# Kernel tuning notes

Hardware: AMD Instinct MI355X
Metric: run time of the kernel (lower is better)

## Reference

```python
import jax, jax.numpy as jnp
import numpy as np

Q_CHAN = 8          # q_chan
IN_CHAN = 128
KS = 56             # kernel_size; ks*ks must equal h*w
STRIDE = 2
BN_EPS = 1e-5


def setup_inputs() -> dict:
    key = jax.random.key(0)
    ks = jax.random.split(key, 10)
    n, c, h, w = 4, IN_CHAN, 56, 56
    hw = h * w  # 3136 == KS*KS
    oc = 4 * Q_CHAN  # qkv conv output channels = 32
    return {
        "x": jax.random.normal(ks[0], (n, c, h, w), dtype=jnp.float32),
        # 1x1 conv weight (out_ch, in_ch) and bias
        "w_qkv": jax.random.normal(ks[1], (oc, c), dtype=jnp.float32) * (1.0 / np.sqrt(c)),
        "b_qkv": jnp.zeros((oc,), dtype=jnp.float32),
        # BatchNorm (inference mode) affine + running stats
        "bn_gamma": jnp.ones((oc,), dtype=jnp.float32),
        "bn_beta": jnp.zeros((oc,), dtype=jnp.float32),
        "bn_mean": jnp.zeros((oc,), dtype=jnp.float32),
        "bn_var": jnp.ones((oc,), dtype=jnp.float32),
        # learned relative position biases, trailing dim = ks*ks = h*w
        "rq": jax.random.normal(ks[2], (Q_CHAN, KS * KS), dtype=jnp.float32),
        "rk": jax.random.normal(ks[3], (Q_CHAN, KS * KS), dtype=jnp.float32),
        "rv": jax.random.normal(ks[4], (2 * Q_CHAN, KS * KS), dtype=jnp.float32),
    }


def reference(x, w_qkv, b_qkv, bn_gamma, bn_beta, bn_mean, bn_var, rq, rk, rv):
    n, c, h, w = x.shape
    # 1x1 conv + inference BatchNorm
    qkv = jnp.einsum('nchw,oc->nohw', x, w_qkv) + b_qkv[None, :, None, None]
    scale = bn_gamma / jnp.sqrt(bn_var + BN_EPS)
    qkv = (qkv - bn_mean[None, :, None, None]) * scale[None, :, None, None] + bn_beta[None, :, None, None]
    qkv = qkv.reshape(n, 4 * Q_CHAN, h * w)
    q = qkv[:, :Q_CHAN]            # [n, 8, hw]
    k = qkv[:, Q_CHAN:2 * Q_CHAN]  # [n, 8, hw]
    v = qkv[:, 2 * Q_CHAN:]        # [n, 16, hw]
    # global attention scores with learned positional bias terms: [n, hw, hw]
    sc = (jnp.einsum('nci,ncj->nij', q, k)
          + jnp.einsum('ci,ncj->nij', rq, q)
          + jnp.einsum('ci,ncj->nij', rk, k))
    sc = jax.nn.softmax(sc, axis=2)
    v = v + rv[None]
    out = jnp.einsum('nij,ncj->nci', sc, v).reshape(n, 2 * Q_CHAN, h, w)
    # AvgPool2d(kernel=stride, stride=stride)
    s = STRIDE
    out = out.reshape(n, 2 * Q_CHAN, h // s, s, w // s, s).mean(axis=(3, 5))
    return out
```

## Files before the change

### kernel.cpp

```cpp
#include <hip/hip_runtime.h>

#define HW 3136
#define CIN 128
#define MHAT 40.0f
#define NSEV 7
#define LOG2E 1.44269504088896340736f
#define NEGC  (-57.7078018f)

typedef __attribute__((ext_vector_type(8))) short bf16x8;
typedef __attribute__((ext_vector_type(4))) float f32x4;

__device__ __forceinline__ unsigned cvtpk(float a, float b) {
    unsigned r;
    asm("v_cvt_pk_bf16_f32 %0, %1, %2" : "=v"(r) : "v"(a), "v"(b));
    return r;
}
__device__ __forceinline__ float lo2f(unsigned p) { return __uint_as_float(p << 16); }
__device__ __forceinline__ float hi2f(unsigned p) { return __uint_as_float(p & 0xffff0000u); }
__device__ __forceinline__ float exp2_hw(float x) {
    float r;
    asm("v_exp_f32 %0, %1" : "=v"(r) : "v"(x));
    return r;
}

union UF { bf16x8 v; unsigned u[4]; };


__global__ __launch_bounds__(256) void proj_mfma(
    const float* __restrict__ x, const float* __restrict__ w,
    const float* __restrict__ bq, const float* __restrict__ gm,
    const float* __restrict__ bt, const float* __restrict__ mu,
    const float* __restrict__ vr, const float* __restrict__ rq,
    const float* __restrict__ rk, const float* __restrict__ rv,
    short* __restrict__ QKWS, short* __restrict__ ASQB, short* __restrict__ VWS)
{
    const int tid = threadIdx.x;
    const int wv = tid >> 6, lane = tid & 63;
    const int il = lane & 15, q = lane >> 4;
    const int jb = blockIdx.x * 64;
    const int nn = blockIdx.y;
    const int z  = blockIdx.z;
    const int jA = jb + wv * 16 + il;
    const float* xn = x + (size_t)nn * CIN * HW;

    UF xh[4], xl[4];
    #pragma unroll
    for (int s = 0; s < 4; ++s) {
        float xv[8];
        #pragma unroll
        for (int u = 0; u < 8; ++u)
            xv[u] = xn[(size_t)(s * 32 + q * 8 + u) * HW + jA];
        #pragma unroll
        for (int t = 0; t < 4; ++t) {
            unsigned hp = cvtpk(xv[2 * t], xv[2 * t + 1]);
            unsigned lp = cvtpk(xv[2 * t] - lo2f(hp), xv[2 * t + 1] - hi2f(hp));
            xh[s].u[t] = hp;
            xl[s].u[t] = lp;
        }
    }
    UF wh[4], wl[4];
    const float* wp = w + (size_t)(z * 16 + il) * CIN;
    #pragma unroll
    for (int s = 0; s < 4; ++s) {
        float4 f0 = *(const float4*)(wp + s * 32 + q * 8);
        float4 f1 = *(const float4*)(wp + s * 32 + q * 8 + 4);
        float wf[8] = {f0.x, f0.y, f0.z, f0.w, f1.x, f1.y, f1.z, f1.w};
        #pragma unroll
        for (int t = 0; t < 4; ++t) {
            unsigned hp = cvtpk(wf[2 * t], wf[2 * t + 1]);
            unsigned lp = cvtpk(wf[2 * t] - lo2f(hp), wf[2 * t + 1] - hi2f(hp));
            wh[s].u[t] = hp;
            wl[s].u[t] = lp;
        }
    }

    f32x4 a0 = {0.f, 0.f, 0.f, 0.f}, a1 = {0.f, 0.f, 0.f, 0.f};
    if (z == 0) {
        #pragma unroll
        for (int s = 0; s < 4; ++s) a0 = __builtin_amdgcn_mfma_f32_16x16x32_bf16(wh[s].v, xh[s].v, a0, 0, 0, 0);
        #pragma unroll
        for (int s = 0; s < 4; ++s) a1 = __builtin_amdgcn_mfma_f32_16x16x32_bf16(wl[s].v, xh[s].v, a1, 0, 0, 0);
        #pragma unroll
        for (int s = 0; s < 4; ++s) a1 = __builtin_amdgcn_mfma_f32_16x16x32_bf16(wh[s].v, xl[s].v, a1, 0, 0, 0);
    } else {
        #pragma unroll
        for (int s = 0; s < 4; ++s) a0 = __builtin_amdgcn_mfma_f32_16x16x32_bf16(xh[s].v, wh[s].v, a0, 0, 0, 0);
        #pragma unroll
        for (int s = 0; s < 4; ++s) a1 = __builtin_amdgcn_mfma_f32_16x16x32_bf16(xl[s].v, wh[s].v, a1, 0, 0, 0);
        #pragma unroll
        for (int s = 0; s < 4; ++s) a1 = __builtin_amdgcn_mfma_f32_16x16x32_bf16(xh[s].v, wl[s].v, a1, 0, 0, 0);
    }
    const f32x4 d = a0 + a1;

    if (z == 0) {
        const int jj = jA;
        float hv[4], av[4];
        #pragma unroll
        for (int r = 0; r < 4; ++r) {
            const int ch = q * 4 + r;
            const float sc = gm[ch] * rsqrtf(vr[ch] + 1e-5f);
            const float sh = (bq[ch] - mu[ch]) * sc + bt[ch];
            const float val = d[r] * sc + sh;
            hv[r] = val;
            const float a = (ch < 8) ? (val + rk[(size_t)ch * HW + jj])
                                     : rq[(size_t)(ch - 8) * HW + jj];
            av[r] = a * LOG2E;
        }
        short* qrow = QKWS + ((size_t)nn * HW + jj) * 32;
        short* arow = ASQB + ((size_t)nn * HW + jj) * 32;
        const int pb = (q * 4) ^ 8;
        unsigned h01 = cvtpk(hv[0], hv[1]), h23 = cvtpk(hv[2], hv[3]);
        unsigned l01 = cvtpk(hv[0] - lo2f(h01), hv[1] - hi2f(h01));
        unsigned l23 = cvtpk(hv[2] - lo2f(h23), hv[3] - hi2f(h23));
        *(unsigned*)&qrow[pb]          = h01;
        *(unsigned*)&qrow[pb + 2]      = h23;
        *(unsigned*)&qrow[16 + pb]     = l01;
        *(unsigned*)&qrow[16 + pb + 2] = l23;
        unsigned c01 = cvtpk(av[0], av[1]), c23 = cvtpk(av[2], av[3]);
        unsigned e01 = cvtpk(av[0] - lo2f(c01), av[1] - hi2f(c01));
        unsigned e23 = cvtpk(av[2] - lo2f(c23), av[3] - hi2f(c23));
        *(unsigned*)&arow[q * 4]          = c01;
        *(unsigned*)&arow[q * 4 + 2]      = c23;
        *(unsigned*)&arow[16 + q * 4]     = e01;
        *(unsigned*)&arow[16 + q * 4 + 2] = e23;
    } else {
        const int ch = 16 + il;
        const float sc = gm[ch] * rsqrtf(vr[ch] + 1e-5f);
        const float sh = (bq[ch] - mu[ch]) * sc + bt[ch];
        const int jbase = jb + wv * 16 + q * 4;
        float4 rvv = *(const float4*)(rv + (size_t)il * HW + jbase);
        float v0 = d[0] * sc + sh + rvv.x;
        float v1 = d[1] * sc + sh + rvv.y;
        float v2 = d[2] * sc + sh + rvv.z;
        float v3 = d[3] * sc + sh + rvv.w;
        short* vp = VWS + (size_t)(nn * 16 + il) * HW + jbase;
        *(unsigned*)&vp[0] = cvtpk(v0, v1);
        *(unsigned*)&vp[2] = cvtpk(v2, v3);
    }
}

#define JT 224
#define QKS 40
#define VTS 232

__global__ __launch_bounds__(256) void attn_mfma(
    const short* __restrict__ QKWS, const short* __restrict__ ASQB,
    const short* __restrict__ VWS,
    float* __restrict__ ONUM, float* __restrict__ OLS)
{
    __shared__ short QK[JT * QKS];
    __shared__ short VT[16 * VTS];
    __shared__ short PB[4 * 16 * QKS];
    const int tid = threadIdx.x;
    const int wv = tid >> 6, lane = tid & 63;
    const int il = lane & 15, q = lane >> 4;
    const int b   = blockIdx.x;
    const int sev = b / 196;
    const int ig  = b % 196;
    const int nn  = ig / 49;
    const int i0  = (ig % 49) * 64 + wv * 16;

    const bf16x8 bco = *(const bf16x8*)(ASQB + ((size_t)nn * HW + i0 + il) * 32 + q * 8);

    const bf16x8 zero8 = {0, 0, 0, 0, 0, 0, 0, 0};
    const f32x4 DINIT = {NEGC, NEGC, NEGC, NEGC};
    f32x4 outc = {0.f, 0.f, 0.f, 0.f};
    float lsum = 0.f;
    short* prow = &PB[(wv * 16 + il) * QKS];

    const int jb0 = (sev * 2 + 0) * JT;
    const int jb1 = (sev * 2 + 1) * JT;
    const int c_v = tid >> 4, jg = tid & 15;

    int4 qa0, qa1, qa2, qa3;
    unsigned vt0, vt1, vt2, vt3, vt4, vt5, vt6;

    if (tid < JT) {
        const short* src = QKWS + ((size_t)nn * HW + jb0 + tid) * 32;
        qa0 = *(const int4*)(src);
        qa1 = *(const int4*)(src + 8);
        qa2 = *(const int4*)(src + 16);
        qa3 = *(const int4*)(src + 24);
    }
    {
        const unsigned* vs = (const unsigned*)(VWS + (size_t)(nn * 16 + c_v) * HW + jb0 + jg * 14);
        vt0 = vs[0]; vt1 = vs[1]; vt2 = vs[2]; vt3 = vs[3]; vt4 = vs[4]; vt5 = vs[5]; vt6 = vs[6];
    }
    if (tid < JT) {
        short* row = &QK[tid * QKS];
        *(int4*)&row[0]  = qa0;
        *(int4*)&row[8]  = qa1;
        *(int4*)&row[16] = qa2;
        *(int4*)&row[24] = qa3;
    }
    {
        unsigned* vd = (unsigned*)&VT[c_v * VTS + jg * 14];
        vd[0] = vt0; vd[1] = vt1; vd[2] = vt2; vd[3] = vt3; vd[4] = vt4; vd[5] = vt5; vd[6] = vt6;
    }
    __syncthreads();

    if (tid < JT) {
        const short* src = QKWS + ((size_t)nn * HW + jb1 + tid) * 32;
        qa0 = *(const int4*)(src);
        qa1 = *(const int4*)(src + 8);
        qa2 = *(const int4*)(src + 16);
        qa3 = *(const int4*)(src + 24);
    }
    {
        const unsigned* vs = (const unsigned*)(VWS + (size_t)(nn * 16 + c_v) * HW + jb1 + jg * 14);
        vt0 = vs[0]; vt1 = vs[1]; vt2 = vs[2]; vt3 = vs[3]; vt4 = vs[4]; vt5 = vs[5]; vt6 = vs[6];
    }

    auto compute14 = [&]() {
        #pragma unroll 2
        for (int step = 0; step < 14; ++step) {
            const short* arow = &QK[(step * 16 + il) * QKS + (q & 1) * 8];
            bf16x8 a1 = *(const bf16x8*)arow;
            bf16x8 a2 = *(const bf16x8*)(arow + 16);
            a2 = (lane < 32) ? a2 : zero8;
            __builtin_amdgcn_s_setprio(1);
            f32x4 d = __builtin_amdgcn_mfma_f32_16x16x32_bf16(a1, bco, DINIT, 0, 0, 0);
            d = __builtin_amdgcn_mfma_f32_16x16x32_bf16(a2, bco, d, 0, 0, 0);
            __builtin_amdgcn_s_setprio(0);
            float p0 = exp2_hw(d[0]), p1 = exp2_hw(d[1]);
            float p2 = exp2_hw(d[2]), p3 = exp2_hw(d[3]);
            lsum += (p0 + p1) + (p2 + p3);
            const int pc = (step & 1) * 16 + q * 4;
            *(unsigned*)&prow[pc]     = cvtpk(p0, p1);
            *(unsigned*)&prow[pc + 2] = cvtpk(p2, p3);
            if (step & 1) {
                bf16x8 ap = *(const bf16x8*)&PB[(wv * 16 + il) * QKS + q * 8];
                bf16x8 bv = *(const bf16x8*)&VT[il * VTS + (step >> 1) * 32 + q * 8];
                __builtin_amdgcn_s_setprio(1);
                outc = __builtin_amdgcn_mfma_f32_16x16x32_bf16(ap, bv, outc, 0, 0, 0);
                __builtin_amdgcn_s_setprio(0);
            }
        }
    };

    compute14();
    __syncthreads();

    if (tid < JT) {
        short* row = &QK[tid * QKS];
        *(int4*)&row[0]  = qa0;
        *(int4*)&row[8]  = qa1;
        *(int4*)&row[16] = qa2;
        *(int4*)&row[24] = qa3;
    }
    {
        unsigned* vd = (unsigned*)&VT[c_v * VTS + jg * 14];
        vd[0] = vt0; vd[1] = vt1; vd[2] = vt2; vd[3] = vt3; vd[4] = vt4; vd[5] = vt5; vd[6] = vt6;
    }
    __syncthreads();

    compute14();

    lsum += __shfl_xor(lsum, 16);
    lsum += __shfl_xor(lsum, 32);
    float* np = ONUM + ((size_t)(sev * 4 + nn) * HW + i0) * 16;
    #pragma unroll
    for (int r = 0; r < 4; ++r)
        np[(q * 4 + r) * 16 + il] = outc[r];
    if (lane < 16)
        OLS[(size_t)(sev * 4 + nn) * HW + i0 + lane] = lsum;
}

__global__ void pool_kernel(const float* __restrict__ ONUM, const float* __restrict__ OLS,
                            float* __restrict__ out) {
    int idx = blockIdx.x * blockDim.x + threadIdx.x;
    if (idx >= 4 * 16 * 28 * 28) return;
    int ow = idx % 28, oh = (idx / 28) % 28;
    int rest = idx / 784;
    int nn = rest >> 4, c = rest & 15;
    float s = 0.f;
    #pragma unroll
    for (int dh = 0; dh < 2; ++dh)
        #pragma unroll
        for (int dw = 0; dw < 2; ++dw) {
            int i = (2 * oh + dh) * 56 + 2 * ow + dw;
            float num = 0.f, l = 0.f;
            #pragma unroll
            for (int p = 0; p < NSEV; ++p) {
                num += ONUM[((size_t)(p * 4 + nn) * HW + i) * 16 + c];
                l   += OLS[(size_t)(p * 4 + nn) * HW + i];
            }
            s += num / l;
        }
    out[idx] = 0.25f * s;
}

#define FJC 392
#define FPSTR 394

__global__ __launch_bounds__(512, 2) void fused_attn(
    const float* __restrict__ x, const float* __restrict__ w,
    const float* __restrict__ bq, const float* __restrict__ gm,
    const float* __restrict__ bt, const float* __restrict__ mu,
    const float* __restrict__ vr, const float* __restrict__ rq,
    const float* __restrict__ rk, const float* __restrict__ rv,
    float* __restrict__ out)
{
    __shared__ float PT[32][FPSTR];
    __shared__ float SQ[56][16];
    __shared__ float ST[56][17];

    const int tid  = threadIdx.x;
    const int wv   = tid >> 6, lane = tid & 63;
    const int bid  = blockIdx.x;
    const int nn   = bid / 56, rem = bid % 56;
    const int oh   = rem >> 1, half = rem & 1;
    const float* xn = x + (size_t)nn * CIN * HW;

    if (tid < 448) {
        int r = tid >> 3, c = tid & 7;
        int rh = (r >= 28) ? 1 : 0, rw = r - 28*rh;
        int i  = (2*oh + rh)*56 + half*28 + rw;
        float acc = 0.f;
        for (int cc = 0; cc < CIN; ++cc)
            acc += xn[cc*HW + i] * w[c*CIN + cc];
        float s  = gm[c] * rsqrtf(vr[c] + 1e-5f);
        float qv = (acc + bq[c] - mu[c])*s + bt[c];
        SQ[r][c]   = qv + rk[c*HW + i];
        SQ[r][8+c] = rq[c*HW + i];
    }

    float l_[7];
    float ac_[7][16];
    #pragma unroll
    for (int r = 0; r < 7; ++r) {
        l_[r] = 0.f;
        #pragma unroll
        for (int c = 0; c < 16; ++c) ac_[r][c] = 0.f;
    }
    __syncthreads();

    for (int cb = 0; cb < 8; ++cb) {
        const int jbase = cb * FJC;
        const int o0 = wv * 4;
        for (int t = 0; t < 4; ++t) {
            int p = lane + 64*t;
            if (p < 196) {
                int j0 = jbase + 2*p;
                float a0x=0.f,a0y=0.f,a1x=0.f,a1y=0.f,a2x=0.f,a2y=0.f,a3x=0.f,a3y=0.f;
                for (int cc = 0; cc < CIN; ++cc) {
                    float2 xv = *(const float2*)(xn + (size_t)cc*HW + j0);
                    float w0 = w[(o0+0)*CIN + cc];
                    float w1 = w[(o0+1)*CIN + cc];
                    float w2 = w[(o0+2)*CIN + cc];
                    float w3 = w[(o0+3)*CIN + cc];
                    a0x += xv.x*w0; a0y += xv.y*w0;
                    a1x += xv.x*w1; a1y += xv.y*w1;
                    a2x += xv.x*w2; a2y += xv.y*w2;
                    a3x += xv.x*w3; a3y += xv.y*w3;
                }
                #pragma unroll
                for (int u = 0; u < 4; ++u) {
                    int o = o0 + u;
                    float av0 = (u==0)? a0x : (u==1)? a1x : (u==2)? a2x : a3x;
                    float av1 = (u==0)? a0y : (u==1)? a1y : (u==2)? a2y : a3y;
                    float s  = gm[o] * rsqrtf(vr[o] + 1e-5f);
                    float sh = (bq[o] - mu[o])*s + bt[o];
                    float v0 = av0*s + sh, v1 = av1*s + sh;
                    if (o >= 16) {
                        v0 += rv[(o-16)*HW + j0];
                        v1 += rv[(o-16)*HW + j0 + 1];
                    }
                    *(float2*)&PT[o][2*p] = make_float2(v0, v1);
                }
            }
        }
        __syncthreads();

        #pragma unroll
        for (int rr = 0; rr < 7; rr += 2) {
            const bool two = (rr + 1) < 7;
            const int ra = wv*7 + rr;
            float A1a[8], A2a[8], A1b[8], A2b[8];
            #pragma unroll
            for (int c = 0; c < 8; ++c) {
                A1a[c] = SQ[ra][c];   A2a[c] = SQ[ra][8+c];
                A1b[c] = two ? SQ[ra+1][c]   : 0.f;
                A2b[c] = two ? SQ[ra+1][8+c] : 0.f;
            }
            for (int t = 0; t < 7; ++t) {
                int jl = 64*t + lane;
                if (jl < FJC) {
                    float qv[8], kv[8], vv[16];
                    #pragma unroll
                    for (int c = 0; c < 8; ++c) { qv[c] = PT[c][jl]; kv[c] = PT[8+c][jl]; }
                    #pragma unroll
                    for (int c = 0; c < 16; ++c) vv[c] = PT[16+c][jl];
                    float sa = 0.f, sb = 0.f;
                    #pragma unroll
                    for (int c = 0; c < 8; ++c) {
                        sa += A1a[c]*kv[c] + A2a[c]*qv[c];
                        sb += A1b[c]*kv[c] + A2b[c]*qv[c];
                    }
                    float pa = __expf(sa - MHAT);
                    l_[rr] += pa;
                    #pragma unroll
                    for (int c = 0; c < 16; ++c) ac_[rr][c] += pa * vv[c];
                    if (two) {
                        float pb = __expf(sb - MHAT);
                        l_[rr+1] += pb;
                        #pragma unroll
                        for (int c = 0; c < 16; ++c) ac_[rr+1][c] += pb * vv[c];
                    }
                }
            }
        }
        __syncthreads();
    }

    #pragma unroll
    for (int rr = 0; rr < 7; ++rr) {
        int r = wv*7 + rr;
        float l = l_[rr];
        #pragma unroll
        for (int off = 32; off; off >>= 1) l += __shfl_xor(l, off);
        if (lane == 0) ST[r][16] = l;
        #pragma unroll
        for (int c = 0; c < 16; ++c) {
            float a = ac_[rr][c];
            #pragma unroll
            for (int off = 32; off; off >>= 1) a += __shfl_xor(a, off);
            if (lane == c) ST[r][c] = a;
        }
    }
    __syncthreads();

    if (tid < 224) {
        int c = tid & 15, qq = tid >> 4;
        float s = 0.f;
        #pragma unroll
        for (int rh = 0; rh < 2; ++rh)
            #pragma unroll
            for (int dw = 0; dw < 2; ++dw) {
                int r = rh*28 + 2*qq + dw;
                s += ST[r][c] / ST[r][16];
            }
        out[((nn*16 + c)*28 + oh)*28 + half*14 + qq] = 0.25f * s;
    }
}

extern "C" void kernel_launch(void* const* d_in, const int* in_sizes, int n_in,
                              void* d_out, int out_size, void* d_ws, size_t ws_size,
                              hipStream_t stream) {
    const float* x     = (const float*)d_in[0];
    const float* w     = (const float*)d_in[1];
    const float* bq    = (const float*)d_in[2];
    const float* gm    = (const float*)d_in[3];
    const float* bt    = (const float*)d_in[4];
    const float* mu    = (const float*)d_in[5];
    const float* vr    = (const float*)d_in[6];
    const float* rq    = (const float*)d_in[7];
    const float* rk    = (const float*)d_in[8];
    const float* rv    = (const float*)d_in[9];
    float* out = (float*)d_out;

    const size_t ONF = (size_t)NSEV * 4 * HW * 16;
    const size_t OLF = (size_t)NSEV * 4 * HW;
    const size_t QKF = (size_t)4 * HW * 32;
    const size_t VWF = (size_t)4 * 16 * HW;
    const size_t NEED = (ONF + OLF) * sizeof(float) + (2 * QKF + VWF) * sizeof(short);

    if (ws_size >= NEED) {
        float* ONUM = (float*)d_ws;
        float* OLS  = ONUM + ONF;
        short* QKWS = (short*)(OLS + OLF);
        short* ASQB = QKWS + QKF;
        short* VWS  = ASQB + QKF;
        proj_mfma<<<dim3(49, 4, 2), 256, 0, stream>>>(x, w, bq, gm, bt, mu, vr, rq, rk, rv, QKWS, ASQB, VWS);
        attn_mfma<<<dim3(196 * NSEV), 256, 0, stream>>>(QKWS, ASQB, VWS, ONUM, OLS);
        pool_kernel<<<dim3(196), 256, 0, stream>>>(ONUM, OLS, out);
    } else {
        fused_attn<<<dim3(224), dim3(512), 0, stream>>>(x, w, bq, gm, bt, mu, vr, rq, rk, rv, out);
    }
}
```

Before: 107.1 us.

## Merge q/k and v projection per wave, tile ONUM layout, and rewrite pooling

The projection kernel now computes both the q/k and v outputs in a single 64-thread block. Previously these came from separate z-slices, so each x tile was loaded and split into bf16 twice; now it is loaded once. The attention kernel writes its per-tile output accumulators as contiguous 16x16 tiles using vector stores instead of strided scalar stores. The pooling kernel is rewritten to work per output row: it reduces the partial softmax sums in shared memory and reads ONUM with float4 loads in the new tiled layout. The P-buffer store is also merged into one 64-bit write. In exchange, the projection launches more and smaller blocks and each thread holds more registers.

```diff
diff --git a/kernel.cpp b/kernel.cpp
--- a/kernel.cpp
+++ b/kernel.cpp
@@ -26,7 +26,7 @@
 union UF { bf16x8 v; unsigned u[4]; };
 
 
-__global__ __launch_bounds__(256) void proj_mfma(
+__global__ __launch_bounds__(64) void proj_mfma(
     const float* __restrict__ x, const float* __restrict__ w,
     const float* __restrict__ bq, const float* __restrict__ gm,
     const float* __restrict__ bt, const float* __restrict__ mu,
@@ -34,13 +34,11 @@
     const float* __restrict__ rk, const float* __restrict__ rv,
     short* __restrict__ QKWS, short* __restrict__ ASQB, short* __restrict__ VWS)
 {
-    const int tid = threadIdx.x;
-    const int wv = tid >> 6, lane = tid & 63;
+    const int lane = threadIdx.x;
     const int il = lane & 15, q = lane >> 4;
-    const int jb = blockIdx.x * 64;
+    const int jb = blockIdx.x * 16;
     const int nn = blockIdx.y;
-    const int z  = blockIdx.z;
-    const int jA = jb + wv * 16 + il;
+    const int jA = jb + il;
     const float* xn = x + (size_t)nn * CIN * HW;
 
     UF xh[4], xl[4];
@@ -58,41 +56,50 @@
             xl[s].u[t] = lp;
         }
     }
-    UF wh[4], wl[4];
-    const float* wp = w + (size_t)(z * 16 + il) * CIN;
-    #pragma unroll
-    for (int s = 0; s < 4; ++s) {
-        float4 f0 = *(const float4*)(wp + s * 32 + q * 8);
-        float4 f1 = *(const float4*)(wp + s * 32 + q * 8 + 4);
-        float wf[8] = {f0.x, f0.y, f0.z, f0.w, f1.x, f1.y, f1.z, f1.w};
-        #pragma unroll
-        for (int t = 0; t < 4; ++t) {
-            unsigned hp = cvtpk(wf[2 * t], wf[2 * t + 1]);
-            unsigned lp = cvtpk(wf[2 * t] - lo2f(hp), wf[2 * t + 1] - hi2f(hp));
-            wh[s].u[t] = hp;
-            wl[s].u[t] = lp;
+    UF wh0[4], wl0[4], wh1[4], wl1[4];
+    {
+        const float* wp0 = w + (size_t)il * CIN;
+        const float* wp1 = w + (size_t)(16 + il) * CIN;
+        #pragma unroll
+        for (int s = 0; s < 4; ++s) {
+            float4 f0 = *(const float4*)(wp0 + s * 32 + q * 8);
+            float4 f1 = *(const float4*)(wp0 + s * 32 + q * 8 + 4);
+            float g0[8] = {f0.x, f0.y, f0.z, f0.w, f1.x, f1.y, f1.z, f1.w};
+            float4 h0 = *(const float4*)(wp1 + s * 32 + q * 8);
+            float4 h1 = *(const float4*)(wp1 + s * 32 + q * 8 + 4);
+            float g1[8] = {h0.x, h0.y, h0.z, h0.w, h1.x, h1.y, h1.z, h1.w};
+            #pragma unroll
+            for (int t = 0; t < 4; ++t) {
+                unsigned hp0 = cvtpk(g0[2 * t], g0[2 * t + 1]);
+                unsigned lp0 = cvtpk(g0[2 * t] - lo2f(hp0), g0[2 * t + 1] - hi2f(hp0));
+                wh0[s].u[t] = hp0;
+                wl0[s].u[t] = lp0;
+                unsigned hp1 = cvtpk(g1[2 * t], g1[2 * t + 1]);
+                unsigned lp1 = cvtpk(g1[2 * t] - lo2f(hp1), g1[2 * t + 1] - hi2f(hp1));
+                wh1[s].u[t] = hp1;
+                wl1[s].u[t] = lp1;
+            }
         }
     }
 
     f32x4 a0 = {0.f, 0.f, 0.f, 0.f}, a1 = {0.f, 0.f, 0.f, 0.f};
-    if (z == 0) {
-        #pragma unroll
-        for (int s = 0; s < 4; ++s) a0 = __builtin_amdgcn_mfma_f32_16x16x32_bf16(wh[s].v, xh[s].v, a0, 0, 0, 0);
-        #pragma unroll
-        for (int s = 0; s < 4; ++s) a1 = __builtin_amdgcn_mfma_f32_16x16x32_bf16(wl[s].v, xh[s].v, a1, 0, 0, 0);
-        #pragma unroll
-        for (int s = 0; s < 4; ++s) a1 = __builtin_amdgcn_mfma_f32_16x16x32_bf16(wh[s].v, xl[s].v, a1, 0, 0, 0);
-    } else {
-        #pragma unroll
-        for (int s = 0; s < 4; ++s) a0 = __builtin_amdgcn_mfma_f32_16x16x32_bf16(xh[s].v, wh[s].v, a0, 0, 0, 0);
-        #pragma unroll
-        for (int s = 0; s < 4; ++s) a1 = __builtin_amdgcn_mfma_f32_16x16x32_bf16(xl[s].v, wh[s].v, a1, 0, 0, 0);
-        #pragma unroll
-        for (int s = 0; s < 4; ++s) a1 = __builtin_amdgcn_mfma_f32_16x16x32_bf16(xh[s].v, wl[s].v, a1, 0, 0, 0);
-    }
-    const f32x4 d = a0 + a1;
-
-    if (z == 0) {
+    #pragma unroll
+    for (int s = 0; s < 4; ++s) a0 = __builtin_amdgcn_mfma_f32_16x16x32_bf16(wh0[s].v, xh[s].v, a0, 0, 0, 0);
+    #pragma unroll
+    for (int s = 0; s < 4; ++s) a1 = __builtin_amdgcn_mfma_f32_16x16x32_bf16(wl0[s].v, xh[s].v, a1, 0, 0, 0);
+    #pragma unroll
+    for (int s = 0; s < 4; ++s) a1 = __builtin_amdgcn_mfma_f32_16x16x32_bf16(wh0[s].v, xl[s].v, a1, 0, 0, 0);
+    const f32x4 d0 = a0 + a1;
+    f32x4 b0 = {0.f, 0.f, 0.f, 0.f}, b1 = {0.f, 0.f, 0.f, 0.f};
+    #pragma unroll
+    for (int s = 0; s < 4; ++s) b0 = __builtin_amdgcn_mfma_f32_16x16x32_bf16(xh[s].v, wh1[s].v, b0, 0, 0, 0);
+    #pragma unroll
+    for (int s = 0; s < 4; ++s) b1 = __builtin_amdgcn_mfma_f32_16x16x32_bf16(xl[s].v, wh1[s].v, b1, 0, 0, 0);
+    #pragma unroll
+    for (int s = 0; s < 4; ++s) b1 = __builtin_amdgcn_mfma_f32_16x16x32_bf16(xh[s].v, wl1[s].v, b1, 0, 0, 0);
+    const f32x4 d1 = b0 + b1;
+
+    {
         const int jj = jA;
         float hv[4], av[4];
         #pragma unroll
@@ -100,7 +107,7 @@
             const int ch = q * 4 + r;
             const float sc = gm[ch] * rsqrtf(vr[ch] + 1e-5f);
             const float sh = (bq[ch] - mu[ch]) * sc + bt[ch];
-            const float val = d[r] * sc + sh;
+            const float val = d0[r] * sc + sh;
             hv[r] = val;
             const float a = (ch < 8) ? (val + rk[(size_t)ch * HW + jj])
                                      : rq[(size_t)(ch - 8) * HW + jj];
@@ -123,16 +130,17 @@
         *(unsigned*)&arow[q * 4 + 2]      = c23;
         *(unsigned*)&arow[16 + q * 4]     = e01;
         *(unsigned*)&arow[16 + q * 4 + 2] = e23;
-    } else {
+    }
+    {
         const int ch = 16 + il;
         const float sc = gm[ch] * rsqrtf(vr[ch] + 1e-5f);
         const float sh = (bq[ch] - mu[ch]) * sc + bt[ch];
-        const int jbase = jb + wv * 16 + q * 4;
+        const int jbase = jb + q * 4;
         float4 rvv = *(const float4*)(rv + (size_t)il * HW + jbase);
-        float v0 = d[0] * sc + sh + rvv.x;
-        float v1 = d[1] * sc + sh + rvv.y;
-        float v2 = d[2] * sc + sh + rvv.z;
-        float v3 = d[3] * sc + sh + rvv.w;
+        float v0 = d1[0] * sc + sh + rvv.x;
+        float v1 = d1[1] * sc + sh + rvv.y;
+        float v2 = d1[2] * sc + sh + rvv.z;
+        float v3 = d1[3] * sc + sh + rvv.w;
         short* vp = VWS + (size_t)(nn * 16 + il) * HW + jbase;
         *(unsigned*)&vp[0] = cvtpk(v0, v1);
         *(unsigned*)&vp[2] = cvtpk(v2, v3);
@@ -158,7 +166,8 @@
     const int sev = b / 196;
     const int ig  = b % 196;
     const int nn  = ig / 49;
-    const int i0  = (ig % 49) * 64 + wv * 16;
+    const int tile = (ig % 49) * 4 + wv;
+    const int i0  = tile * 16;
 
     const bf16x8 bco = *(const bf16x8*)(ASQB + ((size_t)nn * HW + i0 + il) * 32 + q * 8);
 
@@ -226,8 +235,7 @@
             float p2 = exp2_hw(d[2]), p3 = exp2_hw(d[3]);
             lsum += (p0 + p1) + (p2 + p3);
             const int pc = (step & 1) * 16 + q * 4;
-            *(unsigned*)&prow[pc]     = cvtpk(p0, p1);
-            *(unsigned*)&prow[pc + 2] = cvtpk(p2, p3);
+            *(uint2*)&prow[pc] = make_uint2(cvtpk(p0, p1), cvtpk(p2, p3));
             if (step & 1) {
                 bf16x8 ap = *(const bf16x8*)&PB[(wv * 16 + il) * QKS + q * 8];
                 bf16x8 bv = *(const bf16x8*)&VT[il * VTS + (step >> 1) * 32 + q * 8];
@@ -258,36 +266,56 @@
 
     lsum += __shfl_xor(lsum, 16);
     lsum += __shfl_xor(lsum, 32);
-    float* np = ONUM + ((size_t)(sev * 4 + nn) * HW + i0) * 16;
-    #pragma unroll
-    for (int r = 0; r < 4; ++r)
-        np[(q * 4 + r) * 16 + il] = outc[r];
+    float* np = ONUM + ((size_t)(sev * 4 + nn) * 196 + tile) * 256;
+    *(f32x4*)(np + il * 16 + q * 4) = outc;
     if (lane < 16)
         OLS[(size_t)(sev * 4 + nn) * HW + i0 + lane] = lsum;
 }
 
-__global__ void pool_kernel(const float* __restrict__ ONUM, const float* __restrict__ OLS,
-                            float* __restrict__ out) {
-    int idx = blockIdx.x * blockDim.x + threadIdx.x;
-    if (idx >= 4 * 16 * 28 * 28) return;
-    int ow = idx % 28, oh = (idx / 28) % 28;
-    int rest = idx / 784;
-    int nn = rest >> 4, c = rest & 15;
-    float s = 0.f;
-    #pragma unroll
-    for (int dh = 0; dh < 2; ++dh)
-        #pragma unroll
-        for (int dw = 0; dw < 2; ++dw) {
-            int i = (2 * oh + dh) * 56 + 2 * ow + dw;
-            float num = 0.f, l = 0.f;
-            #pragma unroll
-            for (int p = 0; p < NSEV; ++p) {
-                num += ONUM[((size_t)(p * 4 + nn) * HW + i) * 16 + c];
-                l   += OLS[(size_t)(p * 4 + nn) * HW + i];
-            }
-            s += num / l;
-        }
-    out[idx] = 0.25f * s;
+__global__ __launch_bounds__(256) void pool_kernel(
+    const float* __restrict__ ONUM, const float* __restrict__ OLS,
+    float* __restrict__ out)
+{
+    __shared__ float LI[112];
+    __shared__ float PL[2][16][28];
+    const int tid = threadIdx.x;
+    const int oh  = blockIdx.x;
+    const int nn  = blockIdx.y;
+    const int T0  = 7 * oh;
+
+    if (tid < 112) {
+        float l = 0.f;
+        #pragma unroll
+        for (int p = 0; p < NSEV; ++p)
+            l += OLS[(size_t)(p * 4 + nn) * HW + 112 * oh + tid];
+        LI[tid] = l;
+    }
+    __syncthreads();
+
+    const int c  = tid >> 4;
+    const int u0 = tid & 15;
+    for (int u = u0; u < 28; u += 16) {
+        const int tt = u >> 2, qd = u & 3;
+        const int o  = u * 4;
+        float4 nu = {0.f, 0.f, 0.f, 0.f};
+        #pragma unroll
+        for (int p = 0; p < NSEV; ++p) {
+            const float4 v = *(const float4*)(ONUM +
+                ((size_t)(p * 4 + nn) * 196 + T0 + tt) * 256 + c * 16 + qd * 4);
+            nu.x += v.x; nu.y += v.y; nu.z += v.z; nu.w += v.w;
+        }
+        const float r0 = nu.x / LI[o], r1 = nu.y / LI[o + 1];
+        const float r2 = nu.z / LI[o + 2], r3 = nu.w / LI[o + 3];
+        const int hb = o / 56, wo = o % 56;
+        PL[hb][c][wo >> 1]       = r0 + r1;
+        PL[hb][c][(wo >> 1) + 1] = r2 + r3;
+    }
+    __syncthreads();
+
+    for (int v = tid; v < 448; v += 256) {
+        const int cc = v / 28, wo = v % 28;
+        out[((nn * 16 + cc) * 28 + oh) * 28 + wo] = 0.25f * (PL[0][cc][wo] + PL[1][cc][wo]);
+    }
 }
 
 #define FJC 392
@@ -459,7 +487,7 @@
     const float* rv    = (const float*)d_in[9];
     float* out = (float*)d_out;
 
-    const size_t ONF = (size_t)NSEV * 4 * HW * 16;
+    const size_t ONF = (size_t)NSEV * 4 * 196 * 256;
     const size_t OLF = (size_t)NSEV * 4 * HW;
     const size_t QKF = (size_t)4 * HW * 32;
     const size_t VWF = (size_t)4 * 16 * HW;
@@ -471,9 +499,9 @@
         short* QKWS = (short*)(OLS + OLF);
         short* ASQB = QKWS + QKF;
         short* VWS  = ASQB + QKF;
-        proj_mfma<<<dim3(49, 4, 2), 256, 0, stream>>>(x, w, bq, gm, bt, mu, vr, rq, rk, rv, QKWS, ASQB, VWS);
+        proj_mfma<<<dim3(196, 4), 64, 0, stream>>>(x, w, bq, gm, bt, mu, vr, rq, rk, rv, QKWS, ASQB, VWS);
         attn_mfma<<<dim3(196 * NSEV), 256, 0, stream>>>(QKWS, ASQB, VWS, ONUM, OLS);
-        pool_kernel<<<dim3(196), 256, 0, stream>>>(ONUM, OLS, out);
+        pool_kernel<<<dim3(28, 4), 256, 0, stream>>>(ONUM, OLS, out);
     } else {
         fused_attn<<<dim3(224), dim3(512), 0, stream>>>(x, w, bq, gm, bt, mu, vr, rq, rk, rv, out);
     }
```

Result: faster. 101.4 us (-5.3%).
